# Performance work log

Hardware: AMD Instinct MI355X
Metric: run time of the kernel (lower is better)

Reference implementation:

```python
import jax, jax.numpy as jnp
import numpy as np

N = 20000
E = 320000
HID = 64
HEADS = 4
OUT = 64
NEG_SLOPE = 0.2


def gat_conv(x, src, dst, W, a_src, a_dst, b, heads, out_ch, n_nodes):
    # Linear transform then split heads: [N, heads, out_ch]
    h = (x @ W).reshape(n_nodes, heads, out_ch)
    # Per-node attention logits (PyG GATConv): alpha_i = <h_i, a>
    alpha_s = (h * a_src).sum(-1)  # [N, heads]
    alpha_d = (h * a_dst).sum(-1)  # [N, heads]
    # Edge-wise raw scores e_{j->i} = LeakyReLU(alpha_s[j] + alpha_d[i])
    e = jax.nn.leaky_relu(alpha_s[src] + alpha_d[dst], NEG_SLOPE)  # [E, heads]
    # Segment softmax over incoming edges of each destination node
    m = jax.ops.segment_max(e, dst, num_segments=n_nodes)  # [N, heads]
    ex = jnp.exp(e - m[dst])
    s = jax.ops.segment_sum(ex, dst, num_segments=n_nodes)  # [N, heads]
    alpha = ex / (s[dst] + 1e-16)  # [E, heads]
    # Weighted scatter-add aggregation
    msg = h[src] * alpha[..., None]  # [E, heads, out_ch]
    out = jax.ops.segment_sum(msg, dst, num_segments=n_nodes)
    return out.reshape(n_nodes, heads * out_ch) + b


def setup_inputs() -> dict:
    key = jax.random.key(0)
    ks = jax.random.split(key, 16)
    sc = lambda fi, fo: 1.0 / np.sqrt(fi)
    x = jax.random.normal(ks[0], (N, HID), dtype=jnp.float32)
    edge_index = jax.random.randint(ks[1], (2, E), 0, N, dtype=jnp.int32)
    d = dict(x=x, edge_index=edge_index)
    # layer 1: HID -> HID, HEADS heads (concat)
    d['W1'] = jax.random.normal(ks[2], (HID, HEADS * HID), jnp.float32) * sc(HID, HEADS * HID)
    d['a1s'] = jax.random.normal(ks[3], (HEADS, HID), jnp.float32) * 0.1
    d['a1d'] = jax.random.normal(ks[4], (HEADS, HID), jnp.float32) * 0.1
    d['b1'] = jnp.zeros((HEADS * HID,), jnp.float32)
    # layer 2: HEADS*HID -> HID, HEADS heads (concat)
    d['W2'] = jax.random.normal(ks[5], (HEADS * HID, HEADS * HID), jnp.float32) * sc(HEADS * HID, HEADS * HID)
    d['a2s'] = jax.random.normal(ks[6], (HEADS, HID), jnp.float32) * 0.1
    d['a2d'] = jax.random.normal(ks[7], (HEADS, HID), jnp.float32) * 0.1
    d['b2'] = jnp.zeros((HEADS * HID,), jnp.float32)
    # layer 3: HEADS*HID -> OUT, 1 head
    d['W3'] = jax.random.normal(ks[8], (HEADS * HID, OUT), jnp.float32) * sc(HEADS * HID, OUT)
    d['a3s'] = jax.random.normal(ks[9], (1, OUT), jnp.float32) * 0.1
    d['a3d'] = jax.random.normal(ks[10], (1, OUT), jnp.float32) * 0.1
    d['b3'] = jnp.zeros((OUT,), jnp.float32)
    return d


def reference(x, edge_index, W1, a1s, a1d, b1, W2, a2s, a2d, b2, W3, a3s, a3d, b3):
    src, dst = edge_index[0], edge_index[1]
    h = jax.nn.relu(gat_conv(x, src, dst, W1, a1s, a1d, b1, HEADS, HID, N))
    h = jax.nn.relu(gat_conv(h, src, dst, W2, a2s, a2d, b2, HEADS, HID, N))
    out = gat_conv(h, src, dst, W3, a3s, a3d, b3, 1, OUT, N)
    return out
```

## Files before the change

kernel.cpp:

```cpp
#include <hip/hip_runtime.h>
#include <hip/hip_bf16.h>
#include <hip/hip_fp16.h>
#include <cstdint>

#define HID 64
#define NHEADS 4
#define NEG_SLOPE 0.2f

typedef __attribute__((ext_vector_type(8))) short short8;
typedef __attribute__((ext_vector_type(16))) float f32x16;
typedef unsigned short us;

__device__ __forceinline__ us f2bf(float f) {
    unsigned int u = __float_as_uint(f);
    unsigned int r = (u + 0x7FFFu + ((u >> 16) & 1u)) >> 16;
    return (us)r;
}
__device__ __forceinline__ float bf2f(us h) {
    return __uint_as_float(((unsigned int)h) << 16);
}
__device__ __forceinline__ float leaky(float e) {
    return (e > 0.f) ? e : NEG_SLOPE * e;
}

__global__ void histo_kernel(const int* __restrict__ dst, int* __restrict__ counts, int E) {
    int i = blockIdx.x * blockDim.x + threadIdx.x;
    if (i < E) atomicAdd(&counts[dst[i]], 1);
}

__global__ __launch_bounds__(256) void scanA_kernel(const int* __restrict__ counts,
                                                    int* __restrict__ bsum, int n) {
    const int i = blockIdx.x * 256 + threadIdx.x;
    int v = (i < n) ? counts[i] : 0;
#pragma unroll
    for (int o = 32; o; o >>= 1) v += __shfl_xor(v, o);
    __shared__ int ws[4];
    if ((threadIdx.x & 63) == 0) ws[threadIdx.x >> 6] = v;
    __syncthreads();
    if (threadIdx.x == 0) bsum[blockIdx.x] = ws[0] + ws[1] + ws[2] + ws[3];
}

__global__ __launch_bounds__(256) void scanB_kernel(int* __restrict__ bsum, int nb) {
    __shared__ int sh[256];
    const int t = threadIdx.x;
    const int v = (t < nb) ? bsum[t] : 0;
    sh[t] = v;
    __syncthreads();
    for (int o = 1; o < 256; o <<= 1) {
        int u = (t >= o) ? sh[t - o] : 0;
        __syncthreads();
        sh[t] += u;
        __syncthreads();
    }
    if (t < nb) bsum[t] = sh[t] - v;
}

__global__ __launch_bounds__(256) void scanC_kernel(const int* __restrict__ counts,
                                                    const int* __restrict__ bsum,
                                                    int* __restrict__ offs,
                                                    int* __restrict__ wp, int n) {
    __shared__ int sh[256];
    const int t = threadIdx.x;
    const int i = blockIdx.x * 256 + t;
    const int v = (i < n) ? counts[i] : 0;
    sh[t] = v;
    __syncthreads();
    for (int o = 1; o < 256; o <<= 1) {
        int u = (t >= o) ? sh[t - o] : 0;
        __syncthreads();
        sh[t] += u;
        __syncthreads();
    }
    const int base = bsum[blockIdx.x];
    if (i < n) {
        const int off = base + sh[t] - v;
        offs[i] = off;
        wp[i] = off;
        if (i == n - 1) offs[n] = base + sh[t];
    }
}

__global__ void scatter_kernel(const int* __restrict__ src, const int* __restrict__ dst,
                               int* __restrict__ wp, int* __restrict__ csr, int E) {
    int i = blockIdx.x * blockDim.x + threadIdx.x;
    if (i < E) {
        int d = dst[i];
        int p = atomicAdd(&wp[d], 1);
        csr[p] = src[i];
    }
}

__device__ __forceinline__ void wsplit_one(const float* __restrict__ W, us* __restrict__ WTh,
                                           us* __restrict__ WTl, int K, int OUTC, int i) {
    const int c = i / K;
    const int k = i - c * K;
    const float v = W[(size_t)k * OUTC + c];
    const us h = f2bf(v);
    WTh[i] = h;
    WTl[i] = f2bf(v - bf2f(h));
}

__device__ __forceinline__ void vaprep_one(const float* __restrict__ W,
                                           const float* __restrict__ as,
                                           const float* __restrict__ ad,
                                           us* __restrict__ vh, us* __restrict__ vl,
                                           int K, int OUTC, int H, int i) {
    const int j = i / K;
    const int k = i - j * K;
    const int hh = (j < 4) ? j : j - 4;
    const float* a = (j < 4) ? as : ad;
    float acc = 0.f;
    if (hh < H) {
        for (int c = 0; c < 64; ++c)
            acc += W[(size_t)k * OUTC + hh * 64 + c] * a[hh * 64 + c];
    }
    const us h = f2bf(acc);
    vh[i] = h;
    vl[i] = f2bf(acc - bf2f(h));
}

__global__ __launch_bounds__(256) void prep_kernel(
    const float* W1, const float* W2, const float* W3,
    const float* a1s, const float* a1d, const float* a2s, const float* a2d,
    const float* a3s, const float* a3d,
    us* wt1h, us* wt1l, us* wt2h, us* wt2l, us* wt3h, us* wt3l,
    us* va1h, us* va1l, us* va2h, us* va2l, us* va3h, us* va3l) {
    int idx = blockIdx.x * 256 + threadIdx.x;
    if (idx < 16384) { wsplit_one(W1, wt1h, wt1l, 64, 256, idx); return; }
    idx -= 16384;
    if (idx < 65536) { wsplit_one(W2, wt2h, wt2l, 256, 256, idx); return; }
    idx -= 65536;
    if (idx < 16384) { wsplit_one(W3, wt3h, wt3l, 256, 64, idx); return; }
    idx -= 16384;
    if (idx < 512) { vaprep_one(W1, a1s, a1d, va1h, va1l, 64, 256, 4, idx); return; }
    idx -= 512;
    if (idx < 2048) { vaprep_one(W2, a2s, a2d, va2h, va2l, 256, 256, 4, idx); return; }
    idx -= 2048;
    if (idx < 2048) { vaprep_one(W3, a3s, a3d, va3h, va3l, 256, 64, 1, idx); return; }
}

template <int K, int OUTC, int BN, int HA>
__global__ __launch_bounds__(256) void gemm_mfma_kernel(const float* __restrict__ X,
                                                        const us* __restrict__ WTh,
                                                        const us* __restrict__ WTl,
                                                        const us* __restrict__ vah,
                                                        const us* __restrict__ val,
                                                        _Float16* __restrict__ H16,
                                                        float* __restrict__ alpha_s,
                                                        float* __restrict__ alpha_d, int nrows) {
    constexpr int CGS = BN / 64;
    constexpr int NB = BN / 64;
    constexpr int TPC = 4 / NB;
    __shared__ short Ah[64 * 32];
    __shared__ short Al[64 * 32];
    __shared__ short Bh[BN * 32];
    __shared__ short Bl[BN * 32];
    __shared__ short Vh[8 * 32];
    __shared__ short Vl[8 * 32];

    const int tid = threadIdx.x;
    const int lane = tid & 63;
    const int wid = tid >> 6;
    const int wr = wid >> 1;
    const int wc = wid & 1;
    const int r31 = lane & 31;
    const int khw = lane >> 5;
    const int row0 = blockIdx.x * 64;
    const int c0 = blockIdx.y * BN;
    const bool alpha_blk = (blockIdx.y == 0);
    const bool alpha_wave = alpha_blk && (wc == 0);

    const int ar = tid >> 2;
    const int akq = (tid & 3) * 8;
    const int arow = row0 + ar;
    const bool aok = arow < nrows;

    const int bcol = tid / TPC;
    const int bkb = (tid % TPC) * NB;

    f32x16 acc[CGS];
#pragma unroll
    for (int cg = 0; cg < CGS; ++cg)
#pragma unroll
        for (int r = 0; r < 16; ++r) acc[cg][r] = 0.f;
    f32x16 accv;
#pragma unroll
    for (int r = 0; r < 16; ++r) accv[r] = 0.f;

    for (int k0 = 0; k0 < K; k0 += 32) {
        __syncthreads();
        {
            float4 v0 = make_float4(0.f, 0.f, 0.f, 0.f), v1 = v0;
            if (aok) {
                v0 = *reinterpret_cast<const float4*>(&X[(size_t)arow * K + k0 + akq]);
                v1 = *reinterpret_cast<const float4*>(&X[(size_t)arow * K + k0 + akq + 4]);
            }
            float vs[8] = {v0.x, v0.y, v0.z, v0.w, v1.x, v1.y, v1.z, v1.w};
            short8 hi, lo;
#pragma unroll
            for (int j = 0; j < 8; ++j) {
                us h = f2bf(vs[j]);
                hi[j] = (short)h;
                lo[j] = (short)f2bf(vs[j] - bf2f(h));
            }
            const int blk = (akq >> 3) ^ (ar & 3);
            const int off = ar * 32 + (blk << 3);
            *reinterpret_cast<short8*>(&Ah[off]) = hi;
            *reinterpret_cast<short8*>(&Al[off]) = lo;
        }
        {
            const us* srcH = &WTh[(size_t)(c0 + bcol) * K + k0 + bkb * 8];
            const us* srcL = &WTl[(size_t)(c0 + bcol) * K + k0 + bkb * 8];
#pragma unroll
            for (int b = 0; b < NB; ++b) {
                short8 h = *reinterpret_cast<const short8*>(&srcH[b * 8]);
                short8 l = *reinterpret_cast<const short8*>(&srcL[b * 8]);
                const int blk = (bkb + b) ^ (bcol & 3);
                const int off = bcol * 32 + (blk << 3);
                *reinterpret_cast<short8*>(&Bh[off]) = h;
                *reinterpret_cast<short8*>(&Bl[off]) = l;
            }
        }
        if (alpha_blk && tid < 32) {
            const int col = tid >> 2, kb2 = tid & 3;
            *reinterpret_cast<short8*>(&Vh[col * 32 + kb2 * 8]) =
                *reinterpret_cast<const short8*>(&vah[col * K + k0 + kb2 * 8]);
            *reinterpret_cast<short8*>(&Vl[col * 32 + kb2 * 8]) =
                *reinterpret_cast<const short8*>(&val[col * K + k0 + kb2 * 8]);
        }
        __syncthreads();
#pragma unroll
        for (int ks = 0; ks < 32; ks += 16) {
            const int kb = (ks >> 3) + khw;
            const int aoff = (wr * 32 + r31) * 32 + ((kb ^ (r31 & 3)) << 3);
            short8 ah = *reinterpret_cast<const short8*>(&Ah[aoff]);
            short8 al = *reinterpret_cast<const short8*>(&Al[aoff]);
#pragma unroll
            for (int cg = 0; cg < CGS; ++cg) {
                const int coll = wc * (BN / 2) + cg * 32 + r31;
                const int boff = coll * 32 + ((kb ^ (r31 & 3)) << 3);
                short8 bh = *reinterpret_cast<const short8*>(&Bh[boff]);
                short8 bl = *reinterpret_cast<const short8*>(&Bl[boff]);
                acc[cg] = __builtin_amdgcn_mfma_f32_32x32x16_bf16(ah, bh, acc[cg], 0, 0, 0);
                acc[cg] = __builtin_amdgcn_mfma_f32_32x32x16_bf16(ah, bl, acc[cg], 0, 0, 0);
                acc[cg] = __builtin_amdgcn_mfma_f32_32x32x16_bf16(al, bh, acc[cg], 0, 0, 0);
            }
            if (alpha_wave) {
                short8 vh = {}, vl = {};
                if (r31 < 8) {
                    vh = *reinterpret_cast<const short8*>(&Vh[r31 * 32 + (kb << 3)]);
                    vl = *reinterpret_cast<const short8*>(&Vl[r31 * 32 + (kb << 3)]);
                }
                accv = __builtin_amdgcn_mfma_f32_32x32x16_bf16(ah, vh, accv, 0, 0, 0);
                accv = __builtin_amdgcn_mfma_f32_32x32x16_bf16(ah, vl, accv, 0, 0, 0);
                accv = __builtin_amdgcn_mfma_f32_32x32x16_bf16(al, vh, accv, 0, 0, 0);
            }
        }
    }

#pragma unroll
    for (int cg = 0; cg < CGS; ++cg) {
#pragma unroll
        for (int reg = 0; reg < 16; ++reg) {
            const int row = row0 + wr * 32 + (reg & 3) + 8 * (reg >> 2) + 4 * khw;
            if (row < nrows) {
                const int col = c0 + wc * (BN / 2) + cg * 32 + r31;
                H16[(size_t)row * OUTC + col] = (_Float16)acc[cg][reg];
            }
        }
    }
    if (alpha_wave && r31 < 8) {
        const int hsel = r31 & 3;
        if (hsel < HA) {
            float* dstp = (r31 < 4) ? alpha_s : alpha_d;
#pragma unroll
            for (int reg = 0; reg < 16; ++reg) {
                const int row = row0 + wr * 32 + (reg & 3) + 8 * (reg >> 2) + 4 * khw;
                if (row < nrows) dstp[(size_t)row * HA + hsel] = accv[reg];
            }
        }
    }
}

template <bool RELU>
__global__ __launch_bounds__(64) void maxagg4_kernel(const _Float16* __restrict__ h,
                                                     const float* __restrict__ alpha_s,
                                                     const float* __restrict__ alpha_d,
                                                     const int* __restrict__ offs,
                                                     const int* __restrict__ csr,
                                                     float* __restrict__ w,
                                                     const float* __restrict__ bias,
                                                     float* __restrict__ out, int n_nodes) {
    __shared__ float wsh[64 * 4];
    const int gw = blockIdx.x;
    const int lane = threadIdx.x;
    if (gw >= n_nodes) return;
    const int start = offs[gw];
    const int end = offs[gw + 1];
    const int deg = end - start;
    const float4 ad = *reinterpret_cast<const float4*>(&alpha_d[(size_t)gw * 4]);
    const int head = lane >> 4;
    const int cb = lane << 2;
    float4 r;
    float4 acc = make_float4(0.f, 0.f, 0.f, 0.f);

    if (deg <= 64) {
        const int i = start + lane;
        const bool has = i < end;
        int s_reg = 0;
        float4 e = make_float4(0.f, 0.f, 0.f, 0.f);
        float4 m = make_float4(-INFINITY, -INFINITY, -INFINITY, -INFINITY);
        if (has) {
            s_reg = csr[i];
            const float4 a = *reinterpret_cast<const float4*>(&alpha_s[(size_t)s_reg * 4]);
            e.x = leaky(a.x + ad.x);
            e.y = leaky(a.y + ad.y);
            e.z = leaky(a.z + ad.z);
            e.w = leaky(a.w + ad.w);
            m = e;
        }
#pragma unroll
        for (int o = 32; o; o >>= 1) {
            m.x = fmaxf(m.x, __shfl_xor(m.x, o));
            m.y = fmaxf(m.y, __shfl_xor(m.y, o));
            m.z = fmaxf(m.z, __shfl_xor(m.z, o));
            m.w = fmaxf(m.w, __shfl_xor(m.w, o));
        }
        float4 ex = make_float4(0.f, 0.f, 0.f, 0.f);
        if (has) {
            ex.x = __expf(e.x - m.x);
            ex.y = __expf(e.y - m.y);
            ex.z = __expf(e.z - m.z);
            ex.w = __expf(e.w - m.w);
        }
        float4 sum = ex;
#pragma unroll
        for (int o = 32; o; o >>= 1) {
            sum.x += __shfl_xor(sum.x, o);
            sum.y += __shfl_xor(sum.y, o);
            sum.z += __shfl_xor(sum.z, o);
            sum.w += __shfl_xor(sum.w, o);
        }
        r.x = 1.f / (sum.x + 1e-16f);
        r.y = 1.f / (sum.y + 1e-16f);
        r.z = 1.f / (sum.z + 1e-16f);
        r.w = 1.f / (sum.w + 1e-16f);
        *reinterpret_cast<float4*>(&wsh[lane * 4]) = ex;
        const int degr = (deg + 7) & ~7;
        for (int j = 0; j < degr; j += 8) {
#pragma unroll
            for (int u = 0; u < 8; ++u) {
                const int s = __shfl(s_reg, j + u);
                const float wv = wsh[(j + u) * 4 + head];
                const uint2 uv = *reinterpret_cast<const uint2*>(&h[(size_t)s * 256 + cb]);
                const float2 f0 = __half22float2(__builtin_bit_cast(__half2, uv.x));
                const float2 f1 = __half22float2(__builtin_bit_cast(__half2, uv.y));
                acc.x = fmaf(wv, f0.x, acc.x);
                acc.y = fmaf(wv, f0.y, acc.y);
                acc.z = fmaf(wv, f1.x, acc.z);
                acc.w = fmaf(wv, f1.y, acc.w);
            }
        }
    } else {
        float4 m = make_float4(-INFINITY, -INFINITY, -INFINITY, -INFINITY);
        float4 sum = make_float4(0.f, 0.f, 0.f, 0.f);
        for (int i = start + lane; i < end; i += 64) {
            const int s = csr[i];
            const float4 a = *reinterpret_cast<const float4*>(&alpha_s[(size_t)s * 4]);
            float4 e;
            e.x = leaky(a.x + ad.x);
            e.y = leaky(a.y + ad.y);
            e.z = leaky(a.z + ad.z);
            e.w = leaky(a.w + ad.w);
            *reinterpret_cast<float4*>(&w[(size_t)i * 4]) = e;
            m.x = fmaxf(m.x, e.x);
            m.y = fmaxf(m.y, e.y);
            m.z = fmaxf(m.z, e.z);
            m.w = fmaxf(m.w, e.w);
        }
#pragma unroll
        for (int o = 32; o; o >>= 1) {
            m.x = fmaxf(m.x, __shfl_xor(m.x, o));
            m.y = fmaxf(m.y, __shfl_xor(m.y, o));
            m.z = fmaxf(m.z, __shfl_xor(m.z, o));
            m.w = fmaxf(m.w, __shfl_xor(m.w, o));
        }
        for (int i = start + lane; i < end; i += 64) {
            float4 e = *reinterpret_cast<float4*>(&w[(size_t)i * 4]);
            e.x = __expf(e.x - m.x);
            e.y = __expf(e.y - m.y);
            e.z = __expf(e.z - m.z);
            e.w = __expf(e.w - m.w);
            *reinterpret_cast<float4*>(&w[(size_t)i * 4]) = e;
            sum.x += e.x;
            sum.y += e.y;
            sum.z += e.z;
            sum.w += e.w;
        }
#pragma unroll
        for (int o = 32; o; o >>= 1) {
            sum.x += __shfl_xor(sum.x, o);
            sum.y += __shfl_xor(sum.y, o);
            sum.z += __shfl_xor(sum.z, o);
            sum.w += __shfl_xor(sum.w, o);
        }
        r.x = 1.f / (sum.x + 1e-16f);
        r.y = 1.f / (sum.y + 1e-16f);
        r.z = 1.f / (sum.z + 1e-16f);
        r.w = 1.f / (sum.w + 1e-16f);
        for (int i = start; i < end; ++i) {
            const int s = csr[i];
            const float4 w0 = *reinterpret_cast<const float4*>(&w[(size_t)i * 4]);
            const float wv = head == 0 ? w0.x : head == 1 ? w0.y : head == 2 ? w0.z : w0.w;
            const uint2 uv = *reinterpret_cast<const uint2*>(&h[(size_t)s * 256 + cb]);
            const float2 f0 = __half22float2(__builtin_bit_cast(__half2, uv.x));
            const float2 f1 = __half22float2(__builtin_bit_cast(__half2, uv.y));
            acc.x = fmaf(wv, f0.x, acc.x);
            acc.y = fmaf(wv, f0.y, acc.y);
            acc.z = fmaf(wv, f1.x, acc.z);
            acc.w = fmaf(wv, f1.y, acc.w);
        }
    }

    const float rv = head == 0 ? r.x : head == 1 ? r.y : head == 2 ? r.z : r.w;
    const float4 b4 = *reinterpret_cast<const float4*>(&bias[cb]);
    float4 o;
    o.x = acc.x * rv + b4.x;
    o.y = acc.y * rv + b4.y;
    o.z = acc.z * rv + b4.z;
    o.w = acc.w * rv + b4.w;
    if (RELU) {
        o.x = fmaxf(o.x, 0.f);
        o.y = fmaxf(o.y, 0.f);
        o.z = fmaxf(o.z, 0.f);
        o.w = fmaxf(o.w, 0.f);
    }
    *reinterpret_cast<float4*>(&out[(size_t)gw * 256 + cb]) = o;
}

template <bool RELU>
__global__ __launch_bounds__(64) void maxagg1_kernel(const _Float16* __restrict__ h,
                                                     const float* __restrict__ alpha_s,
                                                     const float* __restrict__ alpha_d,
                                                     const int* __restrict__ offs,
                                                     const int* __restrict__ csr,
                                                     float* __restrict__ w,
                                                     const float* __restrict__ bias,
                                                     float* __restrict__ out, int n_nodes) {
    const int gw = blockIdx.x;
    const int lane = threadIdx.x;
    if (gw >= n_nodes) return;
    const int start = offs[gw];
    const int end = offs[gw + 1];
    const int deg = end - start;
    const float ad = alpha_d[gw];
    float r;
    float acc = 0.f;

    if (deg <= 64) {
        const int i = start + lane;
        const bool has = i < end;
        int s_reg = 0;
        float e = 0.f, m = -INFINITY;
        if (has) {
            s_reg = csr[i];
            e = leaky(alpha_s[s_reg] + ad);
            m = e;
        }
#pragma unroll
        for (int o = 32; o; o >>= 1) m = fmaxf(m, __shfl_xor(m, o));
        float ex = has ? __expf(e - m) : 0.f;
        float sum = ex;
#pragma unroll
        for (int o = 32; o; o >>= 1) sum += __shfl_xor(sum, o);
        r = 1.f / (sum + 1e-16f);
        const int degr = (deg + 7) & ~7;
        for (int j = 0; j < degr; j += 8) {
#pragma unroll
            for (int u = 0; u < 8; ++u) {
                const int s = __shfl(s_reg, j + u);
                const float wv = __shfl(ex, j + u);
                acc = fmaf(wv, (float)h[(size_t)s * 64 + lane], acc);
            }
        }
    } else {
        float m = -INFINITY, sum = 0.f;
        for (int i = start + lane; i < end; i += 64) {
            const float e = leaky(alpha_s[csr[i]] + ad);
            w[i] = e;
            m = fmaxf(m, e);
        }
#pragma unroll
        for (int o = 32; o; o >>= 1) m = fmaxf(m, __shfl_xor(m, o));
        for (int i = start + lane; i < end; i += 64) {
            const float ex = __expf(w[i] - m);
            w[i] = ex;
            sum += ex;
        }
#pragma unroll
        for (int o = 32; o; o >>= 1) sum += __shfl_xor(sum, o);
        r = 1.f / (sum + 1e-16f);
        for (int i = start; i < end; ++i)
            acc = fmaf(w[i], (float)h[(size_t)csr[i] * 64 + lane], acc);
    }
    float o = acc * r + bias[lane];
    if (RELU) o = fmaxf(o, 0.f);
    out[(size_t)gw * 64 + lane] = o;
}

extern "C" void kernel_launch(void* const* d_in, const int* in_sizes, int n_in,
                              void* d_out, int out_size, void* d_ws, size_t ws_size,
                              hipStream_t stream) {
    const float* x   = (const float*)d_in[0];
    const int*   ei  = (const int*)d_in[1];
    const float* W1  = (const float*)d_in[2];
    const float* a1s = (const float*)d_in[3];
    const float* a1d = (const float*)d_in[4];
    const float* b1  = (const float*)d_in[5];
    const float* W2  = (const float*)d_in[6];
    const float* a2s = (const float*)d_in[7];
    const float* a2d = (const float*)d_in[8];
    const float* b2  = (const float*)d_in[9];
    const float* W3  = (const float*)d_in[10];
    const float* a3s = (const float*)d_in[11];
    const float* a3d = (const float*)d_in[12];
    const float* b3  = (const float*)d_in[13];
    float* out = (float*)d_out;

    const int N = in_sizes[0] / HID;
    const int E = in_sizes[1] / 2;
    const int* src = ei;
    const int* dst = ei + E;

    char* p = (char*)d_ws;
    auto alloc = [&](size_t bytes) {
        char* q = p;
        p += (bytes + 255) & ~(size_t)255;
        return q;
    };
    float* bufA = (float*)alloc((size_t)N * 256 * 4);
    float* bufB = (float*)alloc((size_t)N * 256 * 4);
    _Float16* h16 = (_Float16*)alloc((size_t)N * 256 * 2);
    float* alpS = (float*)alloc((size_t)N * NHEADS * 4);
    float* alpD = (float*)alloc((size_t)N * NHEADS * 4);
    float* wbuf = (float*)alloc((size_t)E * NHEADS * 4);
    int* counts = (int*)alloc((size_t)N * 4);
    int* offs   = (int*)alloc((size_t)(N + 1) * 4);
    int* wp     = (int*)alloc((size_t)N * 4);
    int* csr    = (int*)alloc((size_t)E * 4);
    int* bsum   = (int*)alloc((size_t)256 * 4);
    us* wt1h = (us*)alloc((size_t)64 * 256 * 2);
    us* wt1l = (us*)alloc((size_t)64 * 256 * 2);
    us* wt2h = (us*)alloc((size_t)256 * 256 * 2);
    us* wt2l = (us*)alloc((size_t)256 * 256 * 2);
    us* wt3h = (us*)alloc((size_t)256 * 64 * 2);
    us* wt3l = (us*)alloc((size_t)256 * 64 * 2);
    us* va1h = (us*)alloc((size_t)8 * 64 * 2);
    us* va1l = (us*)alloc((size_t)8 * 64 * 2);
    us* va2h = (us*)alloc((size_t)8 * 256 * 2);
    us* va2l = (us*)alloc((size_t)8 * 256 * 2);
    us* va3h = (us*)alloc((size_t)8 * 256 * 2);
    us* va3l = (us*)alloc((size_t)8 * 256 * 2);

    hipMemsetAsync(counts, 0, (size_t)N * 4, stream);
    const int eb = (E + 255) / 256;
    const int nb = (N + 255) / 256;
    histo_kernel<<<eb, 256, 0, stream>>>(dst, counts, E);
    scanA_kernel<<<nb, 256, 0, stream>>>(counts, bsum, N);
    scanB_kernel<<<1, 256, 0, stream>>>(bsum, nb);
    scanC_kernel<<<nb, 256, 0, stream>>>(counts, bsum, offs, wp, N);
    scatter_kernel<<<eb, 256, 0, stream>>>(src, dst, wp, csr, E);

    prep_kernel<<<(102912 + 255) / 256, 256, 0, stream>>>(
        W1, W2, W3, a1s, a1d, a2s, a2d, a3s, a3d,
        wt1h, wt1l, wt2h, wt2l, wt3h, wt3l,
        va1h, va1l, va2h, va2l, va3h, va3l);

    const int gb64 = (N + 63) / 64;

    gemm_mfma_kernel<64, 256, 128, 4><<<dim3(gb64, 2), 256, 0, stream>>>(
        x, wt1h, wt1l, va1h, va1l, h16, alpS, alpD, N);
    maxagg4_kernel<true><<<N, 64, 0, stream>>>(h16, alpS, alpD, offs, csr, wbuf, b1, bufB, N);

    gemm_mfma_kernel<256, 256, 128, 4><<<dim3(gb64, 2), 256, 0, stream>>>(
        bufB, wt2h, wt2l, va2h, va2l, h16, alpS, alpD, N);
    maxagg4_kernel<true><<<N, 64, 0, stream>>>(h16, alpS, alpD, offs, csr, wbuf, b2, bufA, N);

    gemm_mfma_kernel<256, 64, 64, 1><<<dim3(gb64, 1), 256, 0, stream>>>(
        bufA, wt3h, wt3l, va3h, va3l, h16, alpS, alpD, N);
    maxagg1_kernel<false><<<N, 64, 0, stream>>>(h16, alpS, alpD, offs, csr, wbuf, b3, out, N);
}
```

Measured before the change: 167.5 us.

## Split head aggregation across two waves, pack two nodes per block, fuse scan

The 4-head aggregation kernel now uses two waves per node, each owning two heads, so per-lane gathers shrink from 8 to 4 bytes and per-lane register and shuffle work is halved while parallelism doubles. The single-head aggregation kernel packs two nodes per 128-thread block, halving the block count. The separate block-sum scan kernel is folded into scanC, with every block redundantly scanning the block sums, removing one launch. Trade-offs: the edge list and attention logits are loaded and softmax-reduced twice per node, and the gathers are narrower per lane.

Result: slower. 173.4 us (+3.6%).

```diff
diff --git a/kernel.cpp b/kernel.cpp
--- a/kernel.cpp
+++ b/kernel.cpp
@@ -40,27 +40,22 @@
     if (threadIdx.x == 0) bsum[blockIdx.x] = ws[0] + ws[1] + ws[2] + ws[3];
 }
 
-__global__ __launch_bounds__(256) void scanB_kernel(int* __restrict__ bsum, int nb) {
-    __shared__ int sh[256];
-    const int t = threadIdx.x;
-    const int v = (t < nb) ? bsum[t] : 0;
-    sh[t] = v;
-    __syncthreads();
-    for (int o = 1; o < 256; o <<= 1) {
-        int u = (t >= o) ? sh[t - o] : 0;
-        __syncthreads();
-        sh[t] += u;
-        __syncthreads();
-    }
-    if (t < nb) bsum[t] = sh[t] - v;
-}
-
 __global__ __launch_bounds__(256) void scanC_kernel(const int* __restrict__ counts,
                                                     const int* __restrict__ bsum,
                                                     int* __restrict__ offs,
-                                                    int* __restrict__ wp, int n) {
+                                                    int* __restrict__ wp, int n, int nb) {
     __shared__ int sh[256];
+    __shared__ int shb[256];
     const int t = threadIdx.x;
+    shb[t] = (t < nb) ? bsum[t] : 0;
+    __syncthreads();
+    for (int o = 1; o < 256; o <<= 1) {
+        int u = (t >= o) ? shb[t - o] : 0;
+        __syncthreads();
+        shb[t] += u;
+        __syncthreads();
+    }
+    const int base = (blockIdx.x == 0) ? 0 : shb[blockIdx.x - 1];
     const int i = blockIdx.x * 256 + t;
     const int v = (i < n) ? counts[i] : 0;
     sh[t] = v;
@@ -71,7 +66,6 @@
         sh[t] += u;
         __syncthreads();
     }
-    const int base = bsum[blockIdx.x];
     if (i < n) {
         const int off = base + sh[t] - v;
         offs[i] = off;
@@ -283,172 +277,141 @@
 }
 
 template <bool RELU>
-__global__ __launch_bounds__(64) void maxagg4_kernel(const _Float16* __restrict__ h,
-                                                     const float* __restrict__ alpha_s,
-                                                     const float* __restrict__ alpha_d,
-                                                     const int* __restrict__ offs,
-                                                     const int* __restrict__ csr,
-                                                     float* __restrict__ w,
-                                                     const float* __restrict__ bias,
-                                                     float* __restrict__ out, int n_nodes) {
-    __shared__ float wsh[64 * 4];
+__global__ __launch_bounds__(128) void maxagg4_kernel(const _Float16* __restrict__ h,
+                                                      const float* __restrict__ alpha_s,
+                                                      const float* __restrict__ alpha_d,
+                                                      const int* __restrict__ offs,
+                                                      const int* __restrict__ csr,
+                                                      float* __restrict__ w,
+                                                      const float* __restrict__ bias,
+                                                      float* __restrict__ out, int n_nodes) {
+    __shared__ float wsh[2][64 * 2];
     const int gw = blockIdx.x;
-    const int lane = threadIdx.x;
+    const int hp = threadIdx.x >> 6;
+    const int lane = threadIdx.x & 63;
     if (gw >= n_nodes) return;
     const int start = offs[gw];
     const int end = offs[gw + 1];
     const int deg = end - start;
-    const float4 ad = *reinterpret_cast<const float4*>(&alpha_d[(size_t)gw * 4]);
-    const int head = lane >> 4;
-    const int cb = lane << 2;
-    float4 r;
-    float4 acc = make_float4(0.f, 0.f, 0.f, 0.f);
+    const float2 ad = *reinterpret_cast<const float2*>(&alpha_d[(size_t)gw * 4 + hp * 2]);
+    const int sub = lane >> 5;
+    const int col = hp * 64 + lane;
+    float2 r;
+    float2 acc = make_float2(0.f, 0.f);
 
     if (deg <= 64) {
         const int i = start + lane;
         const bool has = i < end;
         int s_reg = 0;
-        float4 e = make_float4(0.f, 0.f, 0.f, 0.f);
-        float4 m = make_float4(-INFINITY, -INFINITY, -INFINITY, -INFINITY);
+        float2 e = make_float2(0.f, 0.f);
+        float2 m = make_float2(-INFINITY, -INFINITY);
         if (has) {
             s_reg = csr[i];
-            const float4 a = *reinterpret_cast<const float4*>(&alpha_s[(size_t)s_reg * 4]);
+            const float2 a = *reinterpret_cast<const float2*>(&alpha_s[(size_t)s_reg * 4 + hp * 2]);
             e.x = leaky(a.x + ad.x);
             e.y = leaky(a.y + ad.y);
-            e.z = leaky(a.z + ad.z);
-            e.w = leaky(a.w + ad.w);
             m = e;
         }
 #pragma unroll
         for (int o = 32; o; o >>= 1) {
             m.x = fmaxf(m.x, __shfl_xor(m.x, o));
             m.y = fmaxf(m.y, __shfl_xor(m.y, o));
-            m.z = fmaxf(m.z, __shfl_xor(m.z, o));
-            m.w = fmaxf(m.w, __shfl_xor(m.w, o));
-        }
-        float4 ex = make_float4(0.f, 0.f, 0.f, 0.f);
+        }
+        float2 ex = make_float2(0.f, 0.f);
         if (has) {
             ex.x = __expf(e.x - m.x);
             ex.y = __expf(e.y - m.y);
-            ex.z = __expf(e.z - m.z);
-            ex.w = __expf(e.w - m.w);
-        }
-        float4 sum = ex;
+        }
+        float2 sum = ex;
 #pragma unroll
         for (int o = 32; o; o >>= 1) {
             sum.x += __shfl_xor(sum.x, o);
             sum.y += __shfl_xor(sum.y, o);
-            sum.z += __shfl_xor(sum.z, o);
-            sum.w += __shfl_xor(sum.w, o);
         }
         r.x = 1.f / (sum.x + 1e-16f);
         r.y = 1.f / (sum.y + 1e-16f);
-        r.z = 1.f / (sum.z + 1e-16f);
-        r.w = 1.f / (sum.w + 1e-16f);
-        *reinterpret_cast<float4*>(&wsh[lane * 4]) = ex;
+        *reinterpret_cast<float2*>(&wsh[hp][lane * 2]) = ex;
         const int degr = (deg + 7) & ~7;
         for (int j = 0; j < degr; j += 8) {
 #pragma unroll
             for (int u = 0; u < 8; ++u) {
                 const int s = __shfl(s_reg, j + u);
-                const float wv = wsh[(j + u) * 4 + head];
-                const uint2 uv = *reinterpret_cast<const uint2*>(&h[(size_t)s * 256 + cb]);
-                const float2 f0 = __half22float2(__builtin_bit_cast(__half2, uv.x));
-                const float2 f1 = __half22float2(__builtin_bit_cast(__half2, uv.y));
-                acc.x = fmaf(wv, f0.x, acc.x);
-                acc.y = fmaf(wv, f0.y, acc.y);
-                acc.z = fmaf(wv, f1.x, acc.z);
-                acc.w = fmaf(wv, f1.y, acc.w);
+                const float wv = wsh[hp][(j + u) * 2 + sub];
+                const unsigned int uv =
+                    *reinterpret_cast<const unsigned int*>(&h[(size_t)s * 256 + col * 2]);
+                const float2 f = __half22float2(__builtin_bit_cast(__half2, uv));
+                acc.x = fmaf(wv, f.x, acc.x);
+                acc.y = fmaf(wv, f.y, acc.y);
             }
         }
     } else {
-        float4 m = make_float4(-INFINITY, -INFINITY, -INFINITY, -INFINITY);
-        float4 sum = make_float4(0.f, 0.f, 0.f, 0.f);
+        float2 m = make_float2(-INFINITY, -INFINITY);
+        float2 sum = make_float2(0.f, 0.f);
         for (int i = start + lane; i < end; i += 64) {
             const int s = csr[i];
-            const float4 a = *reinterpret_cast<const float4*>(&alpha_s[(size_t)s * 4]);
-            float4 e;
+            const float2 a = *reinterpret_cast<const float2*>(&alpha_s[(size_t)s * 4 + hp * 2]);
+            float2 e;
             e.x = leaky(a.x + ad.x);
             e.y = leaky(a.y + ad.y);
-            e.z = leaky(a.z + ad.z);
-            e.w = leaky(a.w + ad.w);
-            *reinterpret_cast<float4*>(&w[(size_t)i * 4]) = e;
+            *reinterpret_cast<float2*>(&w[(size_t)i * 4 + hp * 2]) = e;
             m.x = fmaxf(m.x, e.x);
             m.y = fmaxf(m.y, e.y);
-            m.z = fmaxf(m.z, e.z);
-            m.w = fmaxf(m.w, e.w);
         }
 #pragma unroll
         for (int o = 32; o; o >>= 1) {
             m.x = fmaxf(m.x, __shfl_xor(m.x, o));
             m.y = fmaxf(m.y, __shfl_xor(m.y, o));
-            m.z = fmaxf(m.z, __shfl_xor(m.z, o));
-            m.w = fmaxf(m.w, __shfl_xor(m.w, o));
         }
         for (int i = start + lane; i < end; i += 64) {
-            float4 e = *reinterpret_cast<float4*>(&w[(size_t)i * 4]);
+            float2 e = *reinterpret_cast<float2*>(&w[(size_t)i * 4 + hp * 2]);
             e.x = __expf(e.x - m.x);
             e.y = __expf(e.y - m.y);
-            e.z = __expf(e.z - m.z);
-            e.w = __expf(e.w - m.w);
-            *reinterpret_cast<float4*>(&w[(size_t)i * 4]) = e;
+            *reinterpret_cast<float2*>(&w[(size_t)i * 4 + hp * 2]) = e;
             sum.x += e.x;
             sum.y += e.y;
-            sum.z += e.z;
-            sum.w += e.w;
         }
 #pragma unroll
         for (int o = 32; o; o >>= 1) {
             sum.x += __shfl_xor(sum.x, o);
             sum.y += __shfl_xor(sum.y, o);
-            sum.z += __shfl_xor(sum.z, o);
-            sum.w += __shfl_xor(sum.w, o);
         }
         r.x = 1.f / (sum.x + 1e-16f);
         r.y = 1.f / (sum.y + 1e-16f);
-        r.z = 1.f / (sum.z + 1e-16f);
-        r.w = 1.f / (sum.w + 1e-16f);
         for (int i = start; i < end; ++i) {
             const int s = csr[i];
-            const float4 w0 = *reinterpret_cast<const float4*>(&w[(size_t)i * 4]);
-            const float wv = head == 0 ? w0.x : head == 1 ? w0.y : head == 2 ? w0.z : w0.w;
-            const uint2 uv = *reinterpret_cast<const uint2*>(&h[(size_t)s * 256 + cb]);
-            const float2 f0 = __half22float2(__builtin_bit_cast(__half2, uv.x));
-            const float2 f1 = __half22float2(__builtin_bit_cast(__half2, uv.y));
-            acc.x = fmaf(wv, f0.x, acc.x);
-            acc.y = fmaf(wv, f0.y, acc.y);
-            acc.z = fmaf(wv, f1.x, acc.z);
-            acc.w = fmaf(wv, f1.y, acc.w);
-        }
-    }
-
-    const float rv = head == 0 ? r.x : head == 1 ? r.y : head == 2 ? r.z : r.w;
-    const float4 b4 = *reinterpret_cast<const float4*>(&bias[cb]);
-    float4 o;
-    o.x = acc.x * rv + b4.x;
-    o.y = acc.y * rv + b4.y;
-    o.z = acc.z * rv + b4.z;
-    o.w = acc.w * rv + b4.w;
+            const float2 wv2 = *reinterpret_cast<const float2*>(&w[(size_t)i * 4 + hp * 2]);
+            const float wv = sub == 0 ? wv2.x : wv2.y;
+            const unsigned int uv =
+                *reinterpret_cast<const unsigned int*>(&h[(size_t)s * 256 + col * 2]);
+            const float2 f = __half22float2(__builtin_bit_cast(__half2, uv));
+            acc.x = fmaf(wv, f.x, acc.x);
+            acc.y = fmaf(wv, f.y, acc.y);
+        }
+    }
+
+    const float rv = sub == 0 ? r.x : r.y;
+    const float2 b2 = *reinterpret_cast<const float2*>(&bias[col * 2]);
+    float2 o;
+    o.x = acc.x * rv + b2.x;
+    o.y = acc.y * rv + b2.y;
     if (RELU) {
         o.x = fmaxf(o.x, 0.f);
         o.y = fmaxf(o.y, 0.f);
-        o.z = fmaxf(o.z, 0.f);
-        o.w = fmaxf(o.w, 0.f);
-    }
-    *reinterpret_cast<float4*>(&out[(size_t)gw * 256 + cb]) = o;
+    }
+    *reinterpret_cast<float2*>(&out[(size_t)gw * 256 + col * 2]) = o;
 }
 
 template <bool RELU>
-__global__ __launch_bounds__(64) void maxagg1_kernel(const _Float16* __restrict__ h,
-                                                     const float* __restrict__ alpha_s,
-                                                     const float* __restrict__ alpha_d,
-                                                     const int* __restrict__ offs,
-                                                     const int* __restrict__ csr,
-                                                     float* __restrict__ w,
-                                                     const float* __restrict__ bias,
-                                                     float* __restrict__ out, int n_nodes) {
-    const int gw = blockIdx.x;
-    const int lane = threadIdx.x;
+__global__ __launch_bounds__(128) void maxagg1_kernel(const _Float16* __restrict__ h,
+                                                      const float* __restrict__ alpha_s,
+                                                      const float* __restrict__ alpha_d,
+                                                      const int* __restrict__ offs,
+                                                      const int* __restrict__ csr,
+                                                      float* __restrict__ w,
+                                                      const float* __restrict__ bias,
+                                                      float* __restrict__ out, int n_nodes) {
+    const int gw = blockIdx.x * 2 + (threadIdx.x >> 6);
+    const int lane = threadIdx.x & 63;
     if (gw >= n_nodes) return;
     const int start = offs[gw];
     const int end = offs[gw + 1];
@@ -567,8 +530,7 @@
     const int nb = (N + 255) / 256;
     histo_kernel<<<eb, 256, 0, stream>>>(dst, counts, E);
     scanA_kernel<<<nb, 256, 0, stream>>>(counts, bsum, N);
-    scanB_kernel<<<1, 256, 0, stream>>>(bsum, nb);
-    scanC_kernel<<<nb, 256, 0, stream>>>(counts, bsum, offs, wp, N);
+    scanC_kernel<<<nb, 256, 0, stream>>>(counts, bsum, offs, wp, N, nb);
     scatter_kernel<<<eb, 256, 0, stream>>>(src, dst, wp, csr, E);
 
     prep_kernel<<<(102912 + 255) / 256, 256, 0, stream>>>(
@@ -580,13 +542,13 @@
 
     gemm_mfma_kernel<64, 256, 128, 4><<<dim3(gb64, 2), 256, 0, stream>>>(
         x, wt1h, wt1l, va1h, va1l, h16, alpS, alpD, N);
-    maxagg4_kernel<true><<<N, 64, 0, stream>>>(h16, alpS, alpD, offs, csr, wbuf, b1, bufB, N);
+    maxagg4_kernel<true><<<N, 128, 0, stream>>>(h16, alpS, alpD, offs, csr, wbuf, b1, bufB, N);
 
     gemm_mfma_kernel<256, 256, 128, 4><<<dim3(gb64, 2), 256, 0, stream>>>(
         bufB, wt2h, wt2l, va2h, va2l, h16, alpS, alpD, N);
-    maxagg4_kernel<true><<<N, 64, 0, stream>>>(h16, alpS, alpD, offs, csr, wbuf, b2, bufA, N);
+    maxagg4_kernel<true><<<N, 128, 0, stream>>>(h16, alpS, alpD, offs, csr, wbuf, b2, bufA, N);
 
     gemm_mfma_kernel<256, 64, 64, 1><<<dim3(gb64, 1), 256, 0, stream>>>(
         bufA, wt3h, wt3l, va3h, va3l, h16, alpS, alpD, N);
-    maxagg1_kernel<false><<<N, 64, 0, stream>>>(h16, alpS, alpD, offs, csr, wbuf, b3, out, N);
-}
+    maxagg1_kernel<false><<<(N + 1) / 2, 128, 0, stream>>>(h16, alpS, alpD, offs, csr, wbuf, b3, out, N);
+}
```

## Emit bf16 hi/lo activations from aggregation, widen GEMM K-step, fold scanB into scanC

Applied to the files above, without the earlier changes.

The aggregation kernels now write their ReLU outputs directly as split bf16 hi/lo pairs. The next GEMM therefore loads pre-split operands instead of fp32 and converts nothing in its A-tile load. The input x is split once in the prep kernel. The GEMM stages 64 K-values per sync using doubled shared buffers, halving the barrier count, and the single-block scanB launch is folded into scanC by having each block rescan the block sums. The costs are more shared memory per GEMM block, extra writes of x splits, and redundant block-sum scans in every scanC block.

After: 166.4 us (median of 2 runs). Within noise of the previous version (-0.6%).

```diff
diff --git a/kernel.cpp b/kernel.cpp
--- a/kernel.cpp
+++ b/kernel.cpp
@@ -8,6 +8,7 @@
 #define NEG_SLOPE 0.2f
 
 typedef __attribute__((ext_vector_type(8))) short short8;
+typedef __attribute__((ext_vector_type(4))) short short4v;
 typedef __attribute__((ext_vector_type(16))) float f32x16;
 typedef unsigned short us;
 
@@ -40,27 +41,22 @@
     if (threadIdx.x == 0) bsum[blockIdx.x] = ws[0] + ws[1] + ws[2] + ws[3];
 }
 
-__global__ __launch_bounds__(256) void scanB_kernel(int* __restrict__ bsum, int nb) {
-    __shared__ int sh[256];
-    const int t = threadIdx.x;
-    const int v = (t < nb) ? bsum[t] : 0;
-    sh[t] = v;
-    __syncthreads();
-    for (int o = 1; o < 256; o <<= 1) {
-        int u = (t >= o) ? sh[t - o] : 0;
-        __syncthreads();
-        sh[t] += u;
-        __syncthreads();
-    }
-    if (t < nb) bsum[t] = sh[t] - v;
-}
-
 __global__ __launch_bounds__(256) void scanC_kernel(const int* __restrict__ counts,
                                                     const int* __restrict__ bsum,
                                                     int* __restrict__ offs,
-                                                    int* __restrict__ wp, int n) {
+                                                    int* __restrict__ wp, int n, int nb) {
     __shared__ int sh[256];
+    __shared__ int shb[256];
     const int t = threadIdx.x;
+    shb[t] = (t < nb) ? bsum[t] : 0;
+    __syncthreads();
+    for (int o = 1; o < 256; o <<= 1) {
+        int u = (t >= o) ? shb[t - o] : 0;
+        __syncthreads();
+        shb[t] += u;
+        __syncthreads();
+    }
+    const int base = (blockIdx.x == 0) ? 0 : shb[blockIdx.x - 1];
     const int i = blockIdx.x * 256 + t;
     const int v = (i < n) ? counts[i] : 0;
     sh[t] = v;
@@ -71,7 +67,6 @@
         sh[t] += u;
         __syncthreads();
     }
-    const int base = bsum[blockIdx.x];
     if (i < n) {
         const int off = base + sh[t] - v;
         offs[i] = off;
@@ -120,12 +115,22 @@
 }
 
 __global__ __launch_bounds__(256) void prep_kernel(
+    const float* x, int nx,
     const float* W1, const float* W2, const float* W3,
     const float* a1s, const float* a1d, const float* a2s, const float* a2d,
     const float* a3s, const float* a3d,
+    us* xh, us* xl,
     us* wt1h, us* wt1l, us* wt2h, us* wt2l, us* wt3h, us* wt3l,
     us* va1h, us* va1l, us* va2h, us* va2l, us* va3h, us* va3l) {
     int idx = blockIdx.x * 256 + threadIdx.x;
+    if (idx < nx) {
+        const float v = x[idx];
+        const us h = f2bf(v);
+        xh[idx] = h;
+        xl[idx] = f2bf(v - bf2f(h));
+        return;
+    }
+    idx -= nx;
     if (idx < 16384) { wsplit_one(W1, wt1h, wt1l, 64, 256, idx); return; }
     idx -= 16384;
     if (idx < 65536) { wsplit_one(W2, wt2h, wt2l, 256, 256, idx); return; }
@@ -140,7 +145,8 @@
 }
 
 template <int K, int OUTC, int BN, int HA>
-__global__ __launch_bounds__(256) void gemm_mfma_kernel(const float* __restrict__ X,
+__global__ __launch_bounds__(256) void gemm_mfma_kernel(const us* __restrict__ AH,
+                                                        const us* __restrict__ AL,
                                                         const us* __restrict__ WTh,
                                                         const us* __restrict__ WTl,
                                                         const us* __restrict__ vah,
@@ -151,12 +157,12 @@
     constexpr int CGS = BN / 64;
     constexpr int NB = BN / 64;
     constexpr int TPC = 4 / NB;
-    __shared__ short Ah[64 * 32];
-    __shared__ short Al[64 * 32];
-    __shared__ short Bh[BN * 32];
-    __shared__ short Bl[BN * 32];
-    __shared__ short Vh[8 * 32];
-    __shared__ short Vl[8 * 32];
+    __shared__ short Ah[2 * 64 * 32];
+    __shared__ short Al[2 * 64 * 32];
+    __shared__ short Bh[2 * BN * 32];
+    __shared__ short Bl[2 * BN * 32];
+    __shared__ short Vh[2 * 8 * 32];
+    __shared__ short Vl[2 * 8 * 32];
 
     const int tid = threadIdx.x;
     const int lane = tid & 63;
@@ -171,10 +177,8 @@
     const bool alpha_wave = alpha_blk && (wc == 0);
 
     const int ar = tid >> 2;
-    const int akq = (tid & 3) * 8;
-    const int arow = row0 + ar;
-    const bool aok = arow < nrows;
-
+    const int akb = tid & 3;
+    const bool aok = (row0 + ar) < nrows;
     const int bcol = tid / TPC;
     const int bkb = (tid % TPC) * NB;
 
@@ -187,73 +191,72 @@
 #pragma unroll
     for (int r = 0; r < 16; ++r) accv[r] = 0.f;
 
-    for (int k0 = 0; k0 < K; k0 += 32) {
+    for (int k0 = 0; k0 < K; k0 += 64) {
         __syncthreads();
-        {
-            float4 v0 = make_float4(0.f, 0.f, 0.f, 0.f), v1 = v0;
-            if (aok) {
-                v0 = *reinterpret_cast<const float4*>(&X[(size_t)arow * K + k0 + akq]);
-                v1 = *reinterpret_cast<const float4*>(&X[(size_t)arow * K + k0 + akq + 4]);
-            }
-            float vs[8] = {v0.x, v0.y, v0.z, v0.w, v1.x, v1.y, v1.z, v1.w};
-            short8 hi, lo;
-#pragma unroll
-            for (int j = 0; j < 8; ++j) {
-                us h = f2bf(vs[j]);
-                hi[j] = (short)h;
-                lo[j] = (short)f2bf(vs[j] - bf2f(h));
-            }
-            const int blk = (akq >> 3) ^ (ar & 3);
-            const int off = ar * 32 + (blk << 3);
-            *reinterpret_cast<short8*>(&Ah[off]) = hi;
-            *reinterpret_cast<short8*>(&Al[off]) = lo;
-        }
-        {
-            const us* srcH = &WTh[(size_t)(c0 + bcol) * K + k0 + bkb * 8];
-            const us* srcL = &WTl[(size_t)(c0 + bcol) * K + k0 + bkb * 8];
-#pragma unroll
-            for (int b = 0; b < NB; ++b) {
-                short8 h = *reinterpret_cast<const short8*>(&srcH[b * 8]);
-                short8 l = *reinterpret_cast<const short8*>(&srcL[b * 8]);
-                const int blk = (bkb + b) ^ (bcol & 3);
-                const int off = bcol * 32 + (blk << 3);
-                *reinterpret_cast<short8*>(&Bh[off]) = h;
-                *reinterpret_cast<short8*>(&Bl[off]) = l;
-            }
-        }
-        if (alpha_blk && tid < 32) {
-            const int col = tid >> 2, kb2 = tid & 3;
-            *reinterpret_cast<short8*>(&Vh[col * 32 + kb2 * 8]) =
-                *reinterpret_cast<const short8*>(&vah[col * K + k0 + kb2 * 8]);
-            *reinterpret_cast<short8*>(&Vl[col * 32 + kb2 * 8]) =
-                *reinterpret_cast<const short8*>(&val[col * K + k0 + kb2 * 8]);
+#pragma unroll
+        for (int sub = 0; sub < 2; ++sub) {
+            {
+                short8 h = {}, l = {};
+                if (aok) {
+                    const size_t so = (size_t)(row0 + ar) * K + k0 + sub * 32 + akb * 8;
+                    h = *reinterpret_cast<const short8*>(&AH[so]);
+                    l = *reinterpret_cast<const short8*>(&AL[so]);
+                }
+                const int off = sub * 2048 + ar * 32 + ((akb ^ (ar & 3)) << 3);
+                *reinterpret_cast<short8*>(&Ah[off]) = h;
+                *reinterpret_cast<short8*>(&Al[off]) = l;
+            }
+            {
+                const us* srcH = &WTh[(size_t)(c0 + bcol) * K + k0 + sub * 32];
+                const us* srcL = &WTl[(size_t)(c0 + bcol) * K + k0 + sub * 32];
+#pragma unroll
+                for (int b = 0; b < NB; ++b) {
+                    short8 h = *reinterpret_cast<const short8*>(&srcH[(bkb + b) * 8]);
+                    short8 l = *reinterpret_cast<const short8*>(&srcL[(bkb + b) * 8]);
+                    const int off = sub * BN * 32 + bcol * 32 + (((bkb + b) ^ (bcol & 3)) << 3);
+                    *reinterpret_cast<short8*>(&Bh[off]) = h;
+                    *reinterpret_cast<short8*>(&Bl[off]) = l;
+                }
+            }
+            if (alpha_blk && tid < 32) {
+                const int col = tid >> 2, kb2 = tid & 3;
+                const int off = sub * 256 + col * 32 + kb2 * 8;
+                *reinterpret_cast<short8*>(&Vh[off]) =
+                    *reinterpret_cast<const short8*>(&vah[col * K + k0 + sub * 32 + kb2 * 8]);
+                *reinterpret_cast<short8*>(&Vl[off]) =
+                    *reinterpret_cast<const short8*>(&val[col * K + k0 + sub * 32 + kb2 * 8]);
+            }
         }
         __syncthreads();
 #pragma unroll
-        for (int ks = 0; ks < 32; ks += 16) {
-            const int kb = (ks >> 3) + khw;
-            const int aoff = (wr * 32 + r31) * 32 + ((kb ^ (r31 & 3)) << 3);
-            short8 ah = *reinterpret_cast<const short8*>(&Ah[aoff]);
-            short8 al = *reinterpret_cast<const short8*>(&Al[aoff]);
-#pragma unroll
-            for (int cg = 0; cg < CGS; ++cg) {
-                const int coll = wc * (BN / 2) + cg * 32 + r31;
-                const int boff = coll * 32 + ((kb ^ (r31 & 3)) << 3);
-                short8 bh = *reinterpret_cast<const short8*>(&Bh[boff]);
-                short8 bl = *reinterpret_cast<const short8*>(&Bl[boff]);
-                acc[cg] = __builtin_amdgcn_mfma_f32_32x32x16_bf16(ah, bh, acc[cg], 0, 0, 0);
-                acc[cg] = __builtin_amdgcn_mfma_f32_32x32x16_bf16(ah, bl, acc[cg], 0, 0, 0);
-                acc[cg] = __builtin_amdgcn_mfma_f32_32x32x16_bf16(al, bh, acc[cg], 0, 0, 0);
-            }
-            if (alpha_wave) {
-                short8 vh = {}, vl = {};
-                if (r31 < 8) {
-                    vh = *reinterpret_cast<const short8*>(&Vh[r31 * 32 + (kb << 3)]);
-                    vl = *reinterpret_cast<const short8*>(&Vl[r31 * 32 + (kb << 3)]);
+        for (int sub = 0; sub < 2; ++sub) {
+#pragma unroll
+            for (int ks = 0; ks < 32; ks += 16) {
+                const int kb = (ks >> 3) + khw;
+                const int aoff = sub * 2048 + (wr * 32 + r31) * 32 + ((kb ^ (r31 & 3)) << 3);
+                short8 ah = *reinterpret_cast<const short8*>(&Ah[aoff]);
+                short8 al = *reinterpret_cast<const short8*>(&Al[aoff]);
+#pragma unroll
+                for (int cg = 0; cg < CGS; ++cg) {
+                    const int coll = wc * (BN / 2) + cg * 32 + r31;
+                    const int boff = sub * BN * 32 + coll * 32 + ((kb ^ (r31 & 3)) << 3);
+                    short8 bh = *reinterpret_cast<const short8*>(&Bh[boff]);
+                    short8 bl = *reinterpret_cast<const short8*>(&Bl[boff]);
+                    acc[cg] = __builtin_amdgcn_mfma_f32_32x32x16_bf16(ah, bh, acc[cg], 0, 0, 0);
+                    acc[cg] = __builtin_amdgcn_mfma_f32_32x32x16_bf16(ah, bl, acc[cg], 0, 0, 0);
+                    acc[cg] = __builtin_amdgcn_mfma_f32_32x32x16_bf16(al, bh, acc[cg], 0, 0, 0);
                 }
-                accv = __builtin_amdgcn_mfma_f32_32x32x16_bf16(ah, vh, accv, 0, 0, 0);
-                accv = __builtin_amdgcn_mfma_f32_32x32x16_bf16(ah, vl, accv, 0, 0, 0);
-                accv = __builtin_amdgcn_mfma_f32_32x32x16_bf16(al, vh, accv, 0, 0, 0);
+                if (alpha_wave) {
+                    short8 vh = {}, vl = {};
+                    if (r31 < 8) {
+                        const int voff = sub * 256 + r31 * 32 + (kb << 3);
+                        vh = *reinterpret_cast<const short8*>(&Vh[voff]);
+                        vl = *reinterpret_cast<const short8*>(&Vl[voff]);
+                    }
+                    accv = __builtin_amdgcn_mfma_f32_32x32x16_bf16(ah, vh, accv, 0, 0, 0);
+                    accv = __builtin_amdgcn_mfma_f32_32x32x16_bf16(ah, vl, accv, 0, 0, 0);
+                    accv = __builtin_amdgcn_mfma_f32_32x32x16_bf16(al, vh, accv, 0, 0, 0);
+                }
             }
         }
     }
@@ -282,7 +285,6 @@
     }
 }
 
-template <bool RELU>
 __global__ __launch_bounds__(64) void maxagg4_kernel(const _Float16* __restrict__ h,
                                                      const float* __restrict__ alpha_s,
                                                      const float* __restrict__ alpha_d,
@@ -290,7 +292,8 @@
                                                      const int* __restrict__ csr,
                                                      float* __restrict__ w,
                                                      const float* __restrict__ bias,
-                                                     float* __restrict__ out, int n_nodes) {
+                                                     us* __restrict__ outH,
+                                                     us* __restrict__ outL, int n_nodes) {
     __shared__ float wsh[64 * 4];
     const int gw = blockIdx.x;
     const int lane = threadIdx.x;
@@ -424,21 +427,20 @@
 
     const float rv = head == 0 ? r.x : head == 1 ? r.y : head == 2 ? r.z : r.w;
     const float4 b4 = *reinterpret_cast<const float4*>(&bias[cb]);
-    float4 o;
-    o.x = acc.x * rv + b4.x;
-    o.y = acc.y * rv + b4.y;
-    o.z = acc.z * rv + b4.z;
-    o.w = acc.w * rv + b4.w;
-    if (RELU) {
-        o.x = fmaxf(o.x, 0.f);
-        o.y = fmaxf(o.y, 0.f);
-        o.z = fmaxf(o.z, 0.f);
-        o.w = fmaxf(o.w, 0.f);
-    }
-    *reinterpret_cast<float4*>(&out[(size_t)gw * 256 + cb]) = o;
-}
-
-template <bool RELU>
+    float o0 = fmaxf(acc.x * rv + b4.x, 0.f);
+    float o1 = fmaxf(acc.y * rv + b4.y, 0.f);
+    float o2 = fmaxf(acc.z * rv + b4.z, 0.f);
+    float o3 = fmaxf(acc.w * rv + b4.w, 0.f);
+    short4v oh, ol;
+    us t;
+    t = f2bf(o0); oh[0] = (short)t; ol[0] = (short)f2bf(o0 - bf2f(t));
+    t = f2bf(o1); oh[1] = (short)t; ol[1] = (short)f2bf(o1 - bf2f(t));
+    t = f2bf(o2); oh[2] = (short)t; ol[2] = (short)f2bf(o2 - bf2f(t));
+    t = f2bf(o3); oh[3] = (short)t; ol[3] = (short)f2bf(o3 - bf2f(t));
+    *reinterpret_cast<short4v*>(&outH[(size_t)gw * 256 + cb]) = oh;
+    *reinterpret_cast<short4v*>(&outL[(size_t)gw * 256 + cb]) = ol;
+}
+
 __global__ __launch_bounds__(64) void maxagg1_kernel(const _Float16* __restrict__ h,
                                                      const float* __restrict__ alpha_s,
                                                      const float* __restrict__ alpha_d,
@@ -504,7 +506,6 @@
             acc = fmaf(w[i], (float)h[(size_t)csr[i] * 64 + lane], acc);
     }
     float o = acc * r + bias[lane];
-    if (RELU) o = fmaxf(o, 0.f);
     out[(size_t)gw * 64 + lane] = o;
 }
 
@@ -538,9 +539,13 @@
         p += (bytes + 255) & ~(size_t)255;
         return q;
     };
-    float* bufA = (float*)alloc((size_t)N * 256 * 4);
-    float* bufB = (float*)alloc((size_t)N * 256 * 4);
     _Float16* h16 = (_Float16*)alloc((size_t)N * 256 * 2);
+    us* xh  = (us*)alloc((size_t)N * 64 * 2);
+    us* xl  = (us*)alloc((size_t)N * 64 * 2);
+    us* g1h = (us*)alloc((size_t)N * 256 * 2);
+    us* g1l = (us*)alloc((size_t)N * 256 * 2);
+    us* g2h = (us*)alloc((size_t)N * 256 * 2);
+    us* g2l = (us*)alloc((size_t)N * 256 * 2);
     float* alpS = (float*)alloc((size_t)N * NHEADS * 4);
     float* alpD = (float*)alloc((size_t)N * NHEADS * 4);
     float* wbuf = (float*)alloc((size_t)E * NHEADS * 4);
@@ -567,26 +572,27 @@
     const int nb = (N + 255) / 256;
     histo_kernel<<<eb, 256, 0, stream>>>(dst, counts, E);
     scanA_kernel<<<nb, 256, 0, stream>>>(counts, bsum, N);
-    scanB_kernel<<<1, 256, 0, stream>>>(bsum, nb);
-    scanC_kernel<<<nb, 256, 0, stream>>>(counts, bsum, offs, wp, N);
+    scanC_kernel<<<nb, 256, 0, stream>>>(counts, bsum, offs, wp, N, nb);
     scatter_kernel<<<eb, 256, 0, stream>>>(src, dst, wp, csr, E);
 
-    prep_kernel<<<(102912 + 255) / 256, 256, 0, stream>>>(
-        W1, W2, W3, a1s, a1d, a2s, a2d, a3s, a3d,
-        wt1h, wt1l, wt2h, wt2l, wt3h, wt3l,
+    const int nx = N * 64;
+    const int ptotal = nx + 102912;
+    prep_kernel<<<(ptotal + 255) / 256, 256, 0, stream>>>(
+        x, nx, W1, W2, W3, a1s, a1d, a2s, a2d, a3s, a3d,
+        xh, xl, wt1h, wt1l, wt2h, wt2l, wt3h, wt3l,
         va1h, va1l, va2h, va2l, va3h, va3l);
 
     const int gb64 = (N + 63) / 64;
 
     gemm_mfma_kernel<64, 256, 128, 4><<<dim3(gb64, 2), 256, 0, stream>>>(
-        x, wt1h, wt1l, va1h, va1l, h16, alpS, alpD, N);
-    maxagg4_kernel<true><<<N, 64, 0, stream>>>(h16, alpS, alpD, offs, csr, wbuf, b1, bufB, N);
+        xh, xl, wt1h, wt1l, va1h, va1l, h16, alpS, alpD, N);
+    maxagg4_kernel<<<N, 64, 0, stream>>>(h16, alpS, alpD, offs, csr, wbuf, b1, g1h, g1l, N);
 
     gemm_mfma_kernel<256, 256, 128, 4><<<dim3(gb64, 2), 256, 0, stream>>>(
-        bufB, wt2h, wt2l, va2h, va2l, h16, alpS, alpD, N);
-    maxagg4_kernel<true><<<N, 64, 0, stream>>>(h16, alpS, alpD, offs, csr, wbuf, b2, bufA, N);
+        g1h, g1l, wt2h, wt2l, va2h, va2l, h16, alpS, alpD, N);
+    maxagg4_kernel<<<N, 64, 0, stream>>>(h16, alpS, alpD, offs, csr, wbuf, b2, g2h, g2l, N);
 
     gemm_mfma_kernel<256, 64, 64, 1><<<dim3(gb64, 1), 256, 0, stream>>>(
-        bufA, wt3h, wt3l, va3h, va3l, h16, alpS, alpD, N);
-    maxagg1_kernel<false><<<N, 64, 0, stream>>>(h16, alpS, alpD, offs, csr, wbuf, b3, out, N);
-}
+        g2h, g2l, wt3h, wt3l, va3h, va3l, h16, alpS, alpD, N);
+    maxagg1_kernel<<<N, 64, 0, stream>>>(h16, alpS, alpD, offs, csr, wbuf, b3, out, N);
+}
```
